# Kernel tuning notes

Hardware: AMD Instinct MI355X
Metric: run time of the kernel (lower is better)

## Reference

```python
import jax, jax.numpy as jnp
import numpy as np

N_UP, N_DOWN = 8, 8
N_ELEC = N_UP + N_DOWN
N_NUC = 4
D, K, F, H = 128, 64, 32, 45  # embedding, kernel, dist_feat, w-MLP hidden (log-spaced)
CUTOFF = 10.0
B = 2048


def _pairs(a, b):
    s, r = np.meshgrid(a, b, indexing='ij')
    return s.ravel(), r.ravel()


def _edges():
    up = np.arange(N_UP)
    dn = np.arange(N_UP, N_ELEC)
    su, ru = _pairs(up, up); m = su != ru; su, ru = su[m], ru[m]
    sd, rd = _pairs(dn, dn); m = sd != rd; sd, rd = sd[m], rd[m]
    same_s = np.concatenate([su, sd]); same_r = np.concatenate([ru, rd])
    a1s, a1r = _pairs(up, dn); a2s, a2r = _pairs(dn, up)
    anti_s = np.concatenate([a1s, a2s]); anti_r = np.concatenate([a1r, a2r])
    ne_s = np.repeat(np.arange(N_NUC), N_ELEC)
    ne_r = np.tile(np.arange(N_ELEC), N_NUC)
    return tuple(jnp.asarray(x, jnp.int32) for x in (same_s, same_r, anti_s, anti_r, ne_s, ne_r))


def setup_inputs() -> dict:
    key = jax.random.key(0)
    ks = jax.random.split(key, 10)
    rs = jax.random.normal(ks[0], (B, N_ELEC, 3)) * 2.0
    coords = jax.random.normal(ks[1], (N_NUC, 3)) * 2.0
    X_tab = jax.random.normal(ks[2], (1, D))
    Y_w = jax.random.normal(ks[3], (N_NUC, K)) / np.sqrt(N_NUC)
    wW1 = jax.random.normal(ks[4], (3, 3, F, H)) / np.sqrt(F)
    wb1 = jax.random.normal(ks[5], (3, 3, H)) * 0.1
    wW2 = jax.random.normal(ks[6], (3, 3, H, K)) / np.sqrt(H)
    h0_tab = jax.random.normal(ks[7], (2, 1, K))
    hW = jax.random.normal(ks[8], (2, 2, D, K)) / np.sqrt(D)
    gW = jax.random.normal(ks[9], (3, 3, K, D)) / np.sqrt(K)
    same_s, same_r, anti_s, anti_r, ne_s, ne_r = _edges()
    return dict(rs=rs, coords=coords, X_tab=X_tab, Y_w=Y_w, wW1=wW1, wb1=wb1,
                wW2=wW2, h0_tab=h0_tab, hW=hW, gW=gW,
                same_s=same_s, same_r=same_r, anti_s=anti_s, anti_r=anti_r,
                ne_s=ne_s, ne_r=ne_r)


def _dist_basis(d):
    # DistanceBasis with 'nocusp' envelope: env = d^2 exp(-d), gaussians at mus
    qs = jnp.linspace(0.0, 1.0, F)
    mus = CUTOFF * qs ** 2
    sigmas = (1.0 + CUTOFF * qs) / 7.0
    env = d ** 2 * jnp.exp(-d)
    return env[..., None] * jnp.exp(-((d[..., None] - mus) ** 2) / sigmas ** 2)


def reference(rs, coords, X_tab, Y_w, wW1, wb1, wW2, h0_tab, hW, gW,
              same_s, same_r, anti_s, anti_r, ne_s, ne_r):
    Bn = rs.shape[0]
    spin_idxs = jnp.zeros((N_ELEC,), jnp.int32)  # n_up == n_down -> one spin class
    # per-edge distances (layer-0 update_edges_fn featurizes them once)
    d_same = jnp.linalg.norm(rs[:, same_s] - rs[:, same_r], axis=-1)  # [B,112]
    d_anti = jnp.linalg.norm(rs[:, anti_s] - rs[:, anti_r], axis=-1)  # [B,128]
    d_ne = jnp.linalg.norm(coords[ne_s][None] - rs[:, ne_r], axis=-1)  # [B,64]
    feats = [_dist_basis(d_same), _dist_basis(d_anti), _dist_basis(d_ne)]
    senders = [same_s, anti_s, ne_s]
    receivers = [same_r, anti_r, ne_r]
    elec = X_tab[spin_idxs]  # [N_ELEC, D] electron embedding X(spin_idxs)
    nuc = Y_w                # Y(eye(n_nuc)) == Y_w, [N_NUC, K]
    for l in range(3):
        upd = 0.0
        for j in range(3):  # same, anti, ne
            # w subnet: 2-layer MLP, silu hidden with bias, bias-free linear out
            we = jax.nn.silu(feats[j] @ wW1[l, j] + wb1[l, j]) @ wW2[l, j]  # [B,E,K]
            if j < 2:
                if l == 0:
                    hx = h0_tab[j][spin_idxs][senders[j]]            # [E,K] embed
                else:
                    hx = (elec @ hW[l - 1, j])[:, senders[j]]        # [B,E,K]
                weh = we * hx
            else:
                weh = we * nuc[ne_s][None]                           # [B,E,K]
            # segment_sum scatter into receiver electrons
            z = jnp.zeros((Bn, N_ELEC, K), we.dtype).at[:, receivers[j]].add(weh)
            upd = upd + z @ gW[l, j]                                  # [B,N_ELEC,D]
        elec = elec + upd
    return elec
```

## Files before the change

kernel.cpp:

```cpp
#include <hip/hip_runtime.h>
#include <hip/hip_bf16.h>

#define NE 16
#define NN 4
#define DDIM 128
#define KD 64
#define HD 45

typedef _Float16 half8 __attribute__((ext_vector_type(8)));
typedef _Float16 half4 __attribute__((ext_vector_type(4)));
typedef float floatx4 __attribute__((ext_vector_type(4)));

#define OFF_FLAG_B 0
#define OFF_B1_B   64
#define OFF_XT_B   1792
#define OFF_H0_B   2304
#define OFF_YW_B   2560
#define OFF_W1_B   3072
#define OFF_W2_B   30720
#define OFF_GW_B   104448
#define OFF_HW_B   251904
#define OFF_IND_B  317440

__device__ __forceinline__ float ldf(const void* p, long i, int f32) {
    if (f32) return ((const float*)p)[i];
    unsigned int u = ((unsigned int)((const unsigned short*)p)[i]) << 16;
    return __uint_as_float(u);
}

__global__ void prep2_kernel(const void* w1, const void* b1, const void* w2, const void* h0,
                             const void* hW, const void* gW, const void* Yw, const void* Xt,
                             const void* rs,
                             const int* __restrict__ same_r, const int* __restrict__ anti_r,
                             const int* __restrict__ ne_r, char* wsB) {
    __shared__ int badS;
    if (threadIdx.x == 0) badS = 0;
    __syncthreads();
    {
        const unsigned short* rs16 = (const unsigned short*)rs;
        int bad = 0;
        for (int i = threadIdx.x; i < 2048; i += 256) {
            unsigned int u = ((unsigned int)rs16[i]) << 16;
            float v = __uint_as_float(u);
            if (!(fabsf(v) < 1e6f)) bad = 1;
        }
        if (bad) atomicOr(&badS, 1);
    }
    __syncthreads();
    const int f32 = badS ? 1 : 0;
    if (blockIdx.x == 0 && threadIdx.x == 0) *(int*)(wsB + OFF_FLAG_B) = f32;

    int i = blockIdx.x * 256 + threadIdx.x;
    _Float16* W1F = (_Float16*)(wsB + OFF_W1_B);
    _Float16* W2F = (_Float16*)(wsB + OFF_W2_B);
    _Float16* GWF = (_Float16*)(wsB + OFF_GW_B);
    _Float16* HWF = (_Float16*)(wsB + OFF_HW_B);
    _Float16* INDF= (_Float16*)(wsB + OFF_IND_B);
    float*    B1  = (float*)(wsB + OFF_B1_B);
    float*    XT  = (float*)(wsB + OFF_XT_B);
    _Float16* H0F = (_Float16*)(wsB + OFF_H0_B);
    _Float16* YWF = (_Float16*)(wsB + OFF_YW_B);

    if (i < 13824) {
        int lj = i / 1536, rem = i % 1536;
        int nt = rem >> 9, lane = (rem & 511) >> 3, e = rem & 7;
        int row = ((lane >> 4) << 3) + e;
        int col = (nt << 4) + (lane & 15);
        W1F[i] = (_Float16)((col < 45) ? ldf(w1, lj * 1440 + row * 45 + col, f32) : 0.f);
    }
    if (i < 36864) {
        int lj = i / 4096, rem = i & 4095;
        int nt = rem >> 10, kt = (rem >> 9) & 1, lane = (rem & 511) >> 3, e = rem & 7;
        int row = (kt << 5) + ((lane >> 4) << 3) + e;
        int col = (nt << 4) + (lane & 15);
        W2F[i] = (_Float16)((row < 45) ? ldf(w2, lj * 2880 + row * 64 + col, f32) : 0.f);
    }
    if (i < 73728) {
        int lj = i >> 13, rem = i & 8191;
        int nt = rem >> 10, kt = (rem >> 9) & 1, lane = (rem & 511) >> 3, e = rem & 7;
        int row = (kt << 5) + ((lane >> 4) << 3) + e;
        int col = (nt << 4) + (lane & 15);
        GWF[i] = (_Float16)ldf(gW, lj * 8192 + row * 128 + col, f32);
    }
    if (i < 32768) {
        int lj = i >> 13, rem = i & 8191;
        int nt = rem >> 11, kt = (rem >> 9) & 3, lane = (rem & 511) >> 3, e = rem & 7;
        int row = (kt << 5) + ((lane >> 4) << 3) + e;
        int col = (nt << 4) + (lane & 15);
        HWF[i] = (_Float16)ldf(hW, lj * 8192 + row * 64 + col, f32);
    }
    if (i < 5120) {
        int c = i >> 9, rem = i & 511;
        int ln = rem >> 3, ii = rem & 7;
        int cls = (c < 4) ? 0 : ((c < 8) ? 1 : 2);
        int lc  = c - ((cls == 0) ? 0 : ((cls == 1) ? 4 : 8));
        int qd = ln >> 4, lm = ln & 15;
        int e = lc * 32 + qd * 8 + ii;
        int cnt = (cls == 0) ? 112 : ((cls == 1) ? 128 : 64);
        int r = 255;
        if (e < cnt) r = (cls == 0) ? same_r[e] : ((cls == 1) ? anti_r[e] : ne_r[e]);
        INDF[i] = (r == lm) ? (_Float16)1.0f : (_Float16)0.0f;
    }
    if (i < 432) { int lj = i / 48, n = i % 48; B1[i] = (n < 45) ? ldf(b1, lj * 45 + n, f32) : 0.f; }
    if (i < 128) XT[i] = ldf(Xt, i, f32);
    if (i < 128) H0F[i] = (_Float16)ldf(h0, i, f32);
    if (i < 256) YWF[i] = (_Float16)ldf(Yw, i, f32);
}

__device__ __forceinline__ half8 feat_tile(
    const void* __restrict__ rs, const void* __restrict__ coords,
    int b, int lm, int f32, int tloc, int cls,
    const int* __restrict__ S, const int* __restrict__ R,
    const float* __restrict__ A0, const float* __restrict__ B0, const float* __restrict__ C0)
{
    int le = tloc * 16 + lm;
    int s = S[le], r = R[le];
    long rb = ((long)b * NE + r) * 3;
    float bx = ldf(rs, rb + 0, f32), by = ldf(rs, rb + 1, f32), bz = ldf(rs, rb + 2, f32);
    float ax, ay, az;
    if (cls < 2) {
        long sb = ((long)b * NE + s) * 3;
        ax = ldf(rs, sb + 0, f32); ay = ldf(rs, sb + 1, f32); az = ldf(rs, sb + 2, f32);
    } else {
        ax = ldf(coords, s * 3 + 0, f32); ay = ldf(coords, s * 3 + 1, f32); az = ldf(coords, s * 3 + 2, f32);
    }
    float dx = ax - bx, dy = ay - by, dz = az - bz;
    float d = sqrtf(dx * dx + dy * dy + dz * dz);
    float d2 = d * d;
    half8 a;
    #pragma unroll
    for (int ii = 0; ii < 8; ++ii) {
        float E = fmaf(A0[ii], d2, fmaf(B0[ii], d, C0[ii]));
        a[ii] = (_Float16)(d2 * __expf(E));
    }
    return a;
}

__device__ __forceinline__ void we_tile_weh(
    half8 fa, int lj, int tile,
    const char* __restrict__ wsB, _Float16* __restrict__ hid,
    const _Float16* __restrict__ hxrow,
    const unsigned char* __restrict__ sendC,
    _Float16* __restrict__ wehT,
    int lane, int qd, int lm)
{
    const half8* W1F_lj = (const half8*)(wsB + OFF_W1_B) + lj * 192;
    half8 w0 = W1F_lj[lane], w1v = W1F_lj[64 + lane], w2v = W1F_lj[128 + lane];
    const float* B1 = (const float*)(wsB + OFF_B1_B) + lj * 48;
    float bi0 = B1[lm], bi1 = B1[16 + lm], bi2 = B1[32 + lm];
    floatx4 c0 = {0.f,0.f,0.f,0.f}, c1 = c0, c2 = c0;
    c0 = __builtin_amdgcn_mfma_f32_16x16x32_f16(fa, w0,  c0, 0, 0, 0);
    c1 = __builtin_amdgcn_mfma_f32_16x16x32_f16(fa, w1v, c1, 0, 0, 0);
    c2 = __builtin_amdgcn_mfma_f32_16x16x32_f16(fa, w2v, c2, 0, 0, 0);
    #pragma unroll
    for (int rr = 0; rr < 4; ++rr) {
        int row = qd * 4 + rr;
        int x = (row & 7) << 4;
        float v0 = c0[rr] + bi0, v1 = c1[rr] + bi1, v2 = c2[rr] + bi2;
        v0 = v0 * __builtin_amdgcn_rcpf(1.f + __expf(-v0));
        v1 = v1 * __builtin_amdgcn_rcpf(1.f + __expf(-v1));
        v2 = v2 * __builtin_amdgcn_rcpf(1.f + __expf(-v2));
        char* hb = (char*)hid + row * 128;
        *(_Float16*)(hb + ((lm * 2)      ^ x)) = (_Float16)v0;
        *(_Float16*)(hb + ((32 + lm * 2) ^ x)) = (_Float16)v1;
        *(_Float16*)(hb + ((64 + lm * 2) ^ x)) = (_Float16)v2;
    }
    int xr = (lm & 7) << 4;
    half8 a0 = *(const half8*)((const char*)hid + lm * 128 + ((qd * 16)      ^ xr));
    half8 a1 = *(const half8*)((const char*)hid + lm * 128 + ((64 + qd * 16) ^ xr));

    int sv0 = sendC[tile * 16 + qd * 4 + 0];
    int sv1 = sendC[tile * 16 + qd * 4 + 1];
    int sv2 = sendC[tile * 16 + qd * 4 + 2];
    int sv3 = sendC[tile * 16 + qd * 4 + 3];

    const half8* W2F_lj = (const half8*)(wsB + OFF_W2_B) + lj * 512;
    #pragma unroll
    for (int nt = 0; nt < 4; ++nt) {
        half8 bk0 = W2F_lj[nt * 128 + lane], bk1 = W2F_lj[nt * 128 + 64 + lane];
        floatx4 acc = {0.f,0.f,0.f,0.f};
        acc = __builtin_amdgcn_mfma_f32_16x16x32_f16(a0, bk0, acc, 0, 0, 0);
        acc = __builtin_amdgcn_mfma_f32_16x16x32_f16(a1, bk1, acc, 0, 0, 0);
        const int kc = nt * 16 + lm;
        const int eb = tile * 16 + qd * 4;
        wehT[kc * 136 + eb + 0] = (_Float16)(acc[0] * (float)hxrow[sv0 * 68 + kc]);
        wehT[kc * 136 + eb + 1] = (_Float16)(acc[1] * (float)hxrow[sv1 * 68 + kc]);
        wehT[kc * 136 + eb + 2] = (_Float16)(acc[2] * (float)hxrow[sv2 * 68 + kc]);
        wehT[kc * 136 + eb + 3] = (_Float16)(acc[3] * (float)hxrow[sv3 * 68 + kc]);
    }
}

__device__ __forceinline__ void z_mfma4(
    const _Float16* __restrict__ wehT, const half8* __restrict__ INDF, int c0,
    _Float16* __restrict__ zh, int wv, int qd, int lm, int lane)
{
    const _Float16* base = wehT + (wv * 16 + lm) * 136 + qd * 8;
    floatx4 zD = {0.f,0.f,0.f,0.f};
    zD = __builtin_amdgcn_mfma_f32_16x16x32_f16(*(const half8*)(base +  0), INDF[(c0 + 0) * 64 + lane], zD, 0, 0, 0);
    zD = __builtin_amdgcn_mfma_f32_16x16x32_f16(*(const half8*)(base + 32), INDF[(c0 + 1) * 64 + lane], zD, 0, 0, 0);
    zD = __builtin_amdgcn_mfma_f32_16x16x32_f16(*(const half8*)(base + 64), INDF[(c0 + 2) * 64 + lane], zD, 0, 0, 0);
    zD = __builtin_amdgcn_mfma_f32_16x16x32_f16(*(const half8*)(base + 96), INDF[(c0 + 3) * 64 + lane], zD, 0, 0, 0);
    half4 h;
    #pragma unroll
    for (int i = 0; i < 4; ++i) h[i] = (_Float16)zD[i];
    *(half4*)(zh + lm * 72 + wv * 16 + qd * 4) = h;
}

__device__ __forceinline__ void z_mfma2(
    const _Float16* __restrict__ wehT, const half8* __restrict__ INDF, int c0,
    _Float16* __restrict__ zh, int wv, int qd, int lm, int lane)
{
    const _Float16* base = wehT + (wv * 16 + lm) * 136 + qd * 8;
    floatx4 zD = {0.f,0.f,0.f,0.f};
    zD = __builtin_amdgcn_mfma_f32_16x16x32_f16(*(const half8*)(base +  0), INDF[(c0 + 0) * 64 + lane], zD, 0, 0, 0);
    zD = __builtin_amdgcn_mfma_f32_16x16x32_f16(*(const half8*)(base + 32), INDF[(c0 + 1) * 64 + lane], zD, 0, 0, 0);
    half4 h;
    #pragma unroll
    for (int i = 0; i < 4; ++i) h[i] = (_Float16)zD[i];
    *(half4*)(zh + lm * 72 + wv * 16 + qd * 4) = h;
}

__device__ __forceinline__ void gw_accum(
    int L, int j, int wv, int lane, int qd, int lm,
    const _Float16* __restrict__ zh, const half8* __restrict__ GWF, floatx4 (&eacc)[2])
{
    half8 zf0 = *(const half8*)(zh + lm * 72 + qd * 8);
    half8 zf1 = *(const half8*)(zh + lm * 72 + 32 + qd * 8);
    const half8* G = GWF + (size_t)(L * 3 + j) * 1024;
    #pragma unroll
    for (int u = 0; u < 2; ++u) {
        int t2 = wv * 2 + u;
        eacc[u] = __builtin_amdgcn_mfma_f32_16x16x32_f16(zf0, G[t2 * 128 + lane],      eacc[u], 0, 0, 0);
        eacc[u] = __builtin_amdgcn_mfma_f32_16x16x32_f16(zf1, G[t2 * 128 + 64 + lane], eacc[u], 0, 0, 0);
    }
}

__global__ __launch_bounds__(256, 2)
void fused_kernel(const void* __restrict__ rs, const void* __restrict__ coords,
                  const int* __restrict__ same_s, const int* __restrict__ same_r,
                  const int* __restrict__ anti_s, const int* __restrict__ anti_r,
                  const int* __restrict__ ne_s,   const int* __restrict__ ne_r,
                  const char* __restrict__ wsB, void* __restrict__ out)
{
    const int b = blockIdx.x;
    const int tid = threadIdx.x;
    const int wv = tid >> 6, lane = tid & 63;
    const int qd = lane >> 4, lm = lane & 15;
    const int f32 = *(const int*)(wsB + OFF_FLAG_B);

    __shared__ __align__(16) _Float16 wehT[64 * 136];
    __shared__ __align__(16) _Float16 hidA[4][1024];
    __shared__ __align__(16) _Float16 zhS[16 * 72];
    __shared__ _Float16 hxS[2 * 1088];
    __shared__ _Float16 nucS[4 * 68];
    __shared__ __align__(16) _Float16 elecB[16 * 136];
    __shared__ unsigned char sendPad[384];

    const _Float16* H0F = (const _Float16*)(wsB + OFF_H0_B);
    const _Float16* YWF = (const _Float16*)(wsB + OFF_YW_B);
    const float*    XT  = (const float*)(wsB + OFF_XT_B);
    const half8*    GWF = (const half8*)(wsB + OFF_GW_B);
    const half8*    HWF = (const half8*)(wsB + OFF_HW_B);
    const half8*    INDF= (const half8*)(wsB + OFF_IND_B);

    for (int i = tid; i < 384; i += 256) {
        int cls = i >> 7, pos = i & 127;
        int cnt = (cls == 0) ? 112 : ((cls == 1) ? 128 : 64);
        int s = 0;
        if (pos < cnt) {
            if (cls == 0)      s = same_s[pos];
            else if (cls == 1) s = anti_s[pos];
            else               s = ne_s[pos];
        }
        sendPad[i] = (unsigned char)s;
    }
    for (int i = tid; i < 2048; i += 256)
        hxS[(i >> 10) * 1088 + ((i >> 6) & 15) * 68 + (i & 63)] = H0F[((i >> 10) << 6) + (i & 63)];
    if (tid < 256) nucS[(tid >> 6) * 68 + (tid & 63)] = YWF[tid];
    for (int i = tid; i < 4352; i += 256) ((unsigned int*)wehT)[i] = 0u;
    {
        _Float16* hid = hidA[wv];
        half8 z8 = {0,0,0,0,0,0,0,0};
        *(half8*)(hid + lane * 8) = z8;
        *(half8*)(hid + 512 + lane * 8) = z8;
    }
    __syncthreads();

    half8 fa_s0, fa_s1 = {0,0,0,0,0,0,0,0}, fa_a0, fa_a1, fa_n;
    {
        float A0[8], B0[8], C0[8];
        #pragma unroll
        for (int ii = 0; ii < 8; ++ii) {
            float qf = (float)(qd * 8 + ii) * (1.f / 31.f);
            float mu = 10.f * qf * qf;
            float u = 7.f * __builtin_amdgcn_rcpf(1.f + 10.f * qf);
            float is2 = u * u;
            A0[ii] = -is2;
            B0[ii] = 2.f * mu * is2 - 1.f;
            C0[ii] = -(mu * mu) * is2;
        }
        fa_s0 = feat_tile(rs, coords, b, lm, f32, wv,     0, same_s, same_r, A0, B0, C0);
        if (wv < 3)
        fa_s1 = feat_tile(rs, coords, b, lm, f32, wv + 4, 0, same_s, same_r, A0, B0, C0);
        fa_a0 = feat_tile(rs, coords, b, lm, f32, wv,     1, anti_s, anti_r, A0, B0, C0);
        fa_a1 = feat_tile(rs, coords, b, lm, f32, wv + 4, 1, anti_s, anti_r, A0, B0, C0);
        fa_n  = feat_tile(rs, coords, b, lm, f32, wv,     2, ne_s,   ne_r,   A0, B0, C0);
    }

    floatx4 eacc[2];
    #pragma unroll
    for (int u = 0; u < 2; ++u) {
        float xv = XT[(wv * 2 + u) * 16 + lm];
        eacc[u][0] = xv; eacc[u][1] = xv; eacc[u][2] = xv; eacc[u][3] = xv;
    }

    _Float16* hid = hidA[wv];

    for (int L = 0; L < 3; ++L) {
        const int lj0 = L * 3;
        we_tile_weh(fa_s0, lj0, wv, wsB, hid, hxS, sendPad, wehT, lane, qd, lm);
        if (wv < 3)
        we_tile_weh(fa_s1, lj0, wv + 4, wsB, hid, hxS, sendPad, wehT, lane, qd, lm);
        __syncthreads();
        z_mfma4(wehT, INDF, 0, zhS, wv, qd, lm, lane);
        __syncthreads();
        gw_accum(L, 0, wv, lane, qd, lm, zhS, GWF, eacc);
        we_tile_weh(fa_a0, lj0 + 1, wv,     wsB, hid, hxS + 1088, sendPad + 128, wehT, lane, qd, lm);
        we_tile_weh(fa_a1, lj0 + 1, wv + 4, wsB, hid, hxS + 1088, sendPad + 128, wehT, lane, qd, lm);
        __syncthreads();
        z_mfma4(wehT, INDF, 4, zhS, wv, qd, lm, lane);
        __syncthreads();
        gw_accum(L, 1, wv, lane, qd, lm, zhS, GWF, eacc);
        we_tile_weh(fa_n, lj0 + 2, wv, wsB, hid, nucS, sendPad + 256, wehT, lane, qd, lm);
        __syncthreads();
        z_mfma2(wehT, INDF, 8, zhS, wv, qd, lm, lane);
        __syncthreads();
        gw_accum(L, 2, wv, lane, qd, lm, zhS, GWF, eacc);

        if (L < 2) {
            #pragma unroll
            for (int u = 0; u < 2; ++u) {
                int t2 = wv * 2 + u;
                #pragma unroll
                for (int r = 0; r < 4; ++r)
                    elecB[(qd * 4 + r) * 136 + t2 * 16 + lm] = (_Float16)eacc[u][r];
            }
            __syncthreads();
            half8 ae[4];
            #pragma unroll
            for (int kt = 0; kt < 4; ++kt)
                ae[kt] = *(const half8*)(elecB + lm * 136 + kt * 32 + qd * 8);
            #pragma unroll
            for (int u = 0; u < 2; ++u) {
                int idx = wv * 2 + u;
                int j = idx >> 2, nt = idx & 3;
                floatx4 acc = {0.f,0.f,0.f,0.f};
                #pragma unroll
                for (int kt = 0; kt < 4; ++kt) {
                    half8 g = HWF[(size_t)(((L * 2 + j) * 4 + nt) * 4 + kt) * 64 + lane];
                    acc = __builtin_amdgcn_mfma_f32_16x16x32_f16(ae[kt], g, acc, 0, 0, 0);
                }
                #pragma unroll
                for (int r = 0; r < 4; ++r)
                    hxS[j * 1088 + (qd * 4 + r) * 68 + nt * 16 + lm] = (_Float16)acc[r];
            }
            __syncthreads();
        }
    }

    if (f32) {
        float* o = (float*)out + (size_t)b * 2048;
        #pragma unroll
        for (int u = 0; u < 2; ++u)
            #pragma unroll
            for (int r = 0; r < 4; ++r)
                o[(qd * 4 + r) * 128 + (wv * 2 + u) * 16 + lm] = eacc[u][r];
    } else {
        __hip_bfloat16* o = (__hip_bfloat16*)out + (size_t)b * 2048;
        #pragma unroll
        for (int u = 0; u < 2; ++u)
            #pragma unroll
            for (int r = 0; r < 4; ++r)
                o[(qd * 4 + r) * 128 + (wv * 2 + u) * 16 + lm] = __float2bfloat16(eacc[u][r]);
    }
}

extern "C" void kernel_launch(void* const* d_in, const int* in_sizes, int n_in,
                              void* d_out, int out_size, void* d_ws, size_t ws_size,
                              hipStream_t stream) {
    const void* rs     = d_in[0];
    const void* coords = d_in[1];
    const void* X_tab  = d_in[2];
    const void* Y_w    = d_in[3];
    const void* wW1    = d_in[4];
    const void* wb1    = d_in[5];
    const void* wW2    = d_in[6];
    const void* h0     = d_in[7];
    const void* hW     = d_in[8];
    const void* gW     = d_in[9];
    const int* same_s = (const int*)d_in[10];
    const int* same_r = (const int*)d_in[11];
    const int* anti_s = (const int*)d_in[12];
    const int* anti_r = (const int*)d_in[13];
    const int* ne_s   = (const int*)d_in[14];
    const int* ne_r   = (const int*)d_in[15];
    char* wsB = (char*)d_ws;

    const int Bn = in_sizes[0] / (NE * 3);

    prep2_kernel<<<288, 256, 0, stream>>>(wW1, wb1, wW2, h0, hW, gW, Y_w, X_tab, rs,
                                          same_r, anti_r, ne_r, wsB);
    fused_kernel<<<Bn, 256, 0, stream>>>(rs, coords, same_s, same_r, anti_s, anti_r,
                                         ne_s, ne_r, wsB, d_out);
}
```

Before: 187.0 us.

## Pack hidden and hx operands as half2, fold bias into MFMA accumulator

The MLP bias is now loaded into the MFMA accumulator as its initial value, so the separate bias add goes away. The three silu outputs per row are written to LDS as one packed 8-byte store, which needs the W2 weight rows permuted to match the new interleaved hidden layout. The hx and nucleus tables are stored as packed half2 pairs (k and k+32) with stride 33. This lets the weh product use packed fp16 multiplies and 64-bit LDS stores instead of scalar loads and 16-bit stores. It trades fp32 multiplies for fp16 precision in the we*hx product and adds bit-shuffling ALU work.

```diff
diff --git a/kernel.cpp b/kernel.cpp
--- a/kernel.cpp
+++ b/kernel.cpp
@@ -9,6 +9,8 @@
 
 typedef _Float16 half8 __attribute__((ext_vector_type(8)));
 typedef _Float16 half4 __attribute__((ext_vector_type(4)));
+typedef __fp16 half2v __attribute__((ext_vector_type(2)));
+typedef unsigned uint2v __attribute__((ext_vector_type(2)));
 typedef float floatx4 __attribute__((ext_vector_type(4)));
 
 #define OFF_FLAG_B 0
@@ -71,9 +73,10 @@
     if (i < 36864) {
         int lj = i / 4096, rem = i & 4095;
         int nt = rem >> 10, kt = (rem >> 9) & 1, lane = (rem & 511) >> 3, e = rem & 7;
-        int row = (kt << 5) + ((lane >> 4) << 3) + e;
+        int q = (kt << 5) + ((lane >> 4) << 3) + e;
+        int hsel = q & 3, hrow = hsel * 16 + (q >> 2);
         int col = (nt << 4) + (lane & 15);
-        W2F[i] = (_Float16)((row < 45) ? ldf(w2, lj * 2880 + row * 64 + col, f32) : 0.f);
+        W2F[i] = (_Float16)((hsel < 3 && hrow < 45) ? ldf(w2, lj * 2880 + hrow * 64 + col, f32) : 0.f);
     }
     if (i < 73728) {
         int lj = i >> 13, rem = i & 8191;
@@ -139,7 +142,7 @@
 __device__ __forceinline__ void we_tile_weh(
     half8 fa, int lj, int tile,
     const char* __restrict__ wsB, _Float16* __restrict__ hid,
-    const _Float16* __restrict__ hxrow,
+    const unsigned* __restrict__ hxP,
     const unsigned char* __restrict__ sendC,
     _Float16* __restrict__ wehT,
     int lane, int qd, int lm)
@@ -148,45 +151,69 @@
     half8 w0 = W1F_lj[lane], w1v = W1F_lj[64 + lane], w2v = W1F_lj[128 + lane];
     const float* B1 = (const float*)(wsB + OFF_B1_B) + lj * 48;
     float bi0 = B1[lm], bi1 = B1[16 + lm], bi2 = B1[32 + lm];
-    floatx4 c0 = {0.f,0.f,0.f,0.f}, c1 = c0, c2 = c0;
+    floatx4 c0 = {bi0, bi0, bi0, bi0};
+    floatx4 c1 = {bi1, bi1, bi1, bi1};
+    floatx4 c2 = {bi2, bi2, bi2, bi2};
     c0 = __builtin_amdgcn_mfma_f32_16x16x32_f16(fa, w0,  c0, 0, 0, 0);
     c1 = __builtin_amdgcn_mfma_f32_16x16x32_f16(fa, w1v, c1, 0, 0, 0);
     c2 = __builtin_amdgcn_mfma_f32_16x16x32_f16(fa, w2v, c2, 0, 0, 0);
     #pragma unroll
     for (int rr = 0; rr < 4; ++rr) {
         int row = qd * 4 + rr;
-        int x = (row & 7) << 4;
-        float v0 = c0[rr] + bi0, v1 = c1[rr] + bi1, v2 = c2[rr] + bi2;
+        float v0 = c0[rr], v1 = c1[rr], v2 = c2[rr];
         v0 = v0 * __builtin_amdgcn_rcpf(1.f + __expf(-v0));
         v1 = v1 * __builtin_amdgcn_rcpf(1.f + __expf(-v1));
         v2 = v2 * __builtin_amdgcn_rcpf(1.f + __expf(-v2));
-        char* hb = (char*)hid + row * 128;
-        *(_Float16*)(hb + ((lm * 2)      ^ x)) = (_Float16)v0;
-        *(_Float16*)(hb + ((32 + lm * 2) ^ x)) = (_Float16)v1;
-        *(_Float16*)(hb + ((64 + lm * 2) ^ x)) = (_Float16)v2;
+        half2v plo = __builtin_amdgcn_cvt_pkrtz(v0, v1);
+        half2v phi = __builtin_amdgcn_cvt_pkrtz(v2, 0.f);
+        uint2v pk;
+        pk[0] = __builtin_bit_cast(unsigned, plo);
+        pk[1] = __builtin_bit_cast(unsigned, phi);
+        *(uint2v*)((char*)hid + row * 128 + ((lm * 8) ^ ((row & 7) << 4))) = pk;
     }
     int xr = (lm & 7) << 4;
     half8 a0 = *(const half8*)((const char*)hid + lm * 128 + ((qd * 16)      ^ xr));
     half8 a1 = *(const half8*)((const char*)hid + lm * 128 + ((64 + qd * 16) ^ xr));
 
-    int sv0 = sendC[tile * 16 + qd * 4 + 0];
-    int sv1 = sendC[tile * 16 + qd * 4 + 1];
-    int sv2 = sendC[tile * 16 + qd * 4 + 2];
-    int sv3 = sendC[tile * 16 + qd * 4 + 3];
+    unsigned svw = *(const unsigned*)(sendC + tile * 16 + qd * 4);
+    int sv0 = svw & 255, sv1 = (svw >> 8) & 255, sv2 = (svw >> 16) & 255, sv3 = svw >> 24;
 
     const half8* W2F_lj = (const half8*)(wsB + OFF_W2_B) + lj * 512;
-    #pragma unroll
-    for (int nt = 0; nt < 4; ++nt) {
-        half8 bk0 = W2F_lj[nt * 128 + lane], bk1 = W2F_lj[nt * 128 + 64 + lane];
-        floatx4 acc = {0.f,0.f,0.f,0.f};
-        acc = __builtin_amdgcn_mfma_f32_16x16x32_f16(a0, bk0, acc, 0, 0, 0);
-        acc = __builtin_amdgcn_mfma_f32_16x16x32_f16(a1, bk1, acc, 0, 0, 0);
-        const int kc = nt * 16 + lm;
-        const int eb = tile * 16 + qd * 4;
-        wehT[kc * 136 + eb + 0] = (_Float16)(acc[0] * (float)hxrow[sv0 * 68 + kc]);
-        wehT[kc * 136 + eb + 1] = (_Float16)(acc[1] * (float)hxrow[sv1 * 68 + kc]);
-        wehT[kc * 136 + eb + 2] = (_Float16)(acc[2] * (float)hxrow[sv2 * 68 + kc]);
-        wehT[kc * 136 + eb + 3] = (_Float16)(acc[3] * (float)hxrow[sv3 * 68 + kc]);
+    floatx4 acc0 = {0.f,0.f,0.f,0.f}, acc1 = acc0, acc2 = acc0, acc3 = acc0;
+    acc0 = __builtin_amdgcn_mfma_f32_16x16x32_f16(a0, W2F_lj[      lane], acc0, 0, 0, 0);
+    acc0 = __builtin_amdgcn_mfma_f32_16x16x32_f16(a1, W2F_lj[ 64 + lane], acc0, 0, 0, 0);
+    acc1 = __builtin_amdgcn_mfma_f32_16x16x32_f16(a0, W2F_lj[128 + lane], acc1, 0, 0, 0);
+    acc1 = __builtin_amdgcn_mfma_f32_16x16x32_f16(a1, W2F_lj[192 + lane], acc1, 0, 0, 0);
+    acc2 = __builtin_amdgcn_mfma_f32_16x16x32_f16(a0, W2F_lj[256 + lane], acc2, 0, 0, 0);
+    acc2 = __builtin_amdgcn_mfma_f32_16x16x32_f16(a1, W2F_lj[320 + lane], acc2, 0, 0, 0);
+    acc3 = __builtin_amdgcn_mfma_f32_16x16x32_f16(a0, W2F_lj[384 + lane], acc3, 0, 0, 0);
+    acc3 = __builtin_amdgcn_mfma_f32_16x16x32_f16(a1, W2F_lj[448 + lane], acc3, 0, 0, 0);
+
+    const int eb = tile * 16 + qd * 4;
+    #pragma unroll
+    for (int p = 0; p < 2; ++p) {
+        unsigned ha = hxP[sv0 * 33 + p * 16 + lm];
+        unsigned hb = hxP[sv1 * 33 + p * 16 + lm];
+        unsigned hc = hxP[sv2 * 33 + p * 16 + lm];
+        unsigned hd = hxP[sv3 * 33 + p * 16 + lm];
+        floatx4 aL = p ? acc1 : acc0;
+        floatx4 aH = p ? acc3 : acc2;
+        half2v m0h = __builtin_amdgcn_cvt_pkrtz(aL[0], aH[0]) * __builtin_bit_cast(half2v, ha);
+        half2v m1h = __builtin_amdgcn_cvt_pkrtz(aL[1], aH[1]) * __builtin_bit_cast(half2v, hb);
+        half2v m2h = __builtin_amdgcn_cvt_pkrtz(aL[2], aH[2]) * __builtin_bit_cast(half2v, hc);
+        half2v m3h = __builtin_amdgcn_cvt_pkrtz(aL[3], aH[3]) * __builtin_bit_cast(half2v, hd);
+        unsigned m0 = __builtin_bit_cast(unsigned, m0h);
+        unsigned m1 = __builtin_bit_cast(unsigned, m1h);
+        unsigned m2 = __builtin_bit_cast(unsigned, m2h);
+        unsigned m3 = __builtin_bit_cast(unsigned, m3h);
+        uint2v lo, hi;
+        lo[0] = (m0 & 0xFFFFu) | (m1 << 16);
+        lo[1] = (m2 & 0xFFFFu) | (m3 << 16);
+        hi[0] = (m0 >> 16) | (m1 & 0xFFFF0000u);
+        hi[1] = (m2 >> 16) | (m3 & 0xFFFF0000u);
+        const int klo = p * 16 + lm;
+        *(uint2v*)(wehT + klo * 136 + eb) = lo;
+        *(uint2v*)(wehT + (klo + 32) * 136 + eb) = hi;
     }
 }
 
@@ -251,8 +278,8 @@
     __shared__ __align__(16) _Float16 wehT[64 * 136];
     __shared__ __align__(16) _Float16 hidA[4][1024];
     __shared__ __align__(16) _Float16 zhS[16 * 72];
-    __shared__ _Float16 hxS[2 * 1088];
-    __shared__ _Float16 nucS[4 * 68];
+    __shared__ unsigned hxPall[2 * 528];
+    __shared__ unsigned nucP[4 * 33];
     __shared__ __align__(16) _Float16 elecB[16 * 136];
     __shared__ unsigned char sendPad[384];
 
@@ -274,16 +301,19 @@
         }
         sendPad[i] = (unsigned char)s;
     }
-    for (int i = tid; i < 2048; i += 256)
-        hxS[(i >> 10) * 1088 + ((i >> 6) & 15) * 68 + (i & 63)] = H0F[((i >> 10) << 6) + (i & 63)];
-    if (tid < 256) nucS[(tid >> 6) * 68 + (tid & 63)] = YWF[tid];
+    for (int t = tid; t < 1024; t += 256) {
+        int j = t >> 9, rem = t & 511, s = rem >> 5, i = rem & 31;
+        unsigned lo = ((const unsigned short*)H0F)[j * 64 + i];
+        unsigned hi = ((const unsigned short*)H0F)[j * 64 + 32 + i];
+        hxPall[j * 528 + s * 33 + i] = lo | (hi << 16);
+    }
+    if (tid < 128) {
+        int s = tid >> 5, i = tid & 31;
+        unsigned lo = ((const unsigned short*)YWF)[s * 64 + i];
+        unsigned hi = ((const unsigned short*)YWF)[s * 64 + 32 + i];
+        nucP[s * 33 + i] = lo | (hi << 16);
+    }
     for (int i = tid; i < 4352; i += 256) ((unsigned int*)wehT)[i] = 0u;
-    {
-        _Float16* hid = hidA[wv];
-        half8 z8 = {0,0,0,0,0,0,0,0};
-        *(half8*)(hid + lane * 8) = z8;
-        *(half8*)(hid + 512 + lane * 8) = z8;
-    }
     __syncthreads();
 
     half8 fa_s0, fa_s1 = {0,0,0,0,0,0,0,0}, fa_a0, fa_a1, fa_n;
@@ -318,20 +348,20 @@
 
     for (int L = 0; L < 3; ++L) {
         const int lj0 = L * 3;
-        we_tile_weh(fa_s0, lj0, wv, wsB, hid, hxS, sendPad, wehT, lane, qd, lm);
+        we_tile_weh(fa_s0, lj0, wv, wsB, hid, hxPall, sendPad, wehT, lane, qd, lm);
         if (wv < 3)
-        we_tile_weh(fa_s1, lj0, wv + 4, wsB, hid, hxS, sendPad, wehT, lane, qd, lm);
+        we_tile_weh(fa_s1, lj0, wv + 4, wsB, hid, hxPall, sendPad, wehT, lane, qd, lm);
         __syncthreads();
         z_mfma4(wehT, INDF, 0, zhS, wv, qd, lm, lane);
         __syncthreads();
         gw_accum(L, 0, wv, lane, qd, lm, zhS, GWF, eacc);
-        we_tile_weh(fa_a0, lj0 + 1, wv,     wsB, hid, hxS + 1088, sendPad + 128, wehT, lane, qd, lm);
-        we_tile_weh(fa_a1, lj0 + 1, wv + 4, wsB, hid, hxS + 1088, sendPad + 128, wehT, lane, qd, lm);
+        we_tile_weh(fa_a0, lj0 + 1, wv,     wsB, hid, hxPall + 528, sendPad + 128, wehT, lane, qd, lm);
+        we_tile_weh(fa_a1, lj0 + 1, wv + 4, wsB, hid, hxPall + 528, sendPad + 128, wehT, lane, qd, lm);
         __syncthreads();
         z_mfma4(wehT, INDF, 4, zhS, wv, qd, lm, lane);
         __syncthreads();
         gw_accum(L, 1, wv, lane, qd, lm, zhS, GWF, eacc);
-        we_tile_weh(fa_n, lj0 + 2, wv, wsB, hid, nucS, sendPad + 256, wehT, lane, qd, lm);
+        we_tile_weh(fa_n, lj0 + 2, wv, wsB, hid, nucP, sendPad + 256, wehT, lane, qd, lm);
         __syncthreads();
         z_mfma2(wehT, INDF, 8, zhS, wv, qd, lm, lane);
         __syncthreads();
@@ -346,23 +376,29 @@
                     elecB[(qd * 4 + r) * 136 + t2 * 16 + lm] = (_Float16)eacc[u][r];
             }
             __syncthreads();
-            half8 ae[4];
-            #pragma unroll
-            for (int kt = 0; kt < 4; ++kt)
-                ae[kt] = *(const half8*)(elecB + lm * 136 + kt * 32 + qd * 8);
-            #pragma unroll
-            for (int u = 0; u < 2; ++u) {
-                int idx = wv * 2 + u;
-                int j = idx >> 2, nt = idx & 3;
-                floatx4 acc = {0.f,0.f,0.f,0.f};
+            {
+                half8 ae0 = *(const half8*)(elecB + lm * 136 +  0 + qd * 8);
+                half8 ae1 = *(const half8*)(elecB + lm * 136 + 32 + qd * 8);
+                half8 ae2 = *(const half8*)(elecB + lm * 136 + 64 + qd * 8);
+                half8 ae3 = *(const half8*)(elecB + lm * 136 + 96 + qd * 8);
+                _Float16* hp = (_Float16*)hxPall;
                 #pragma unroll
-                for (int kt = 0; kt < 4; ++kt) {
-                    half8 g = HWF[(size_t)(((L * 2 + j) * 4 + nt) * 4 + kt) * 64 + lane];
-                    acc = __builtin_amdgcn_mfma_f32_16x16x32_f16(ae[kt], g, acc, 0, 0, 0);
+                for (int u = 0; u < 2; ++u) {
+                    int idx = wv * 2 + u;
+                    int j = idx >> 2, nt = idx & 3;
+                    const half8* Bb = HWF + (size_t)(((L * 2 + j) * 4 + nt) * 4) * 64;
+                    floatx4 acc = {0.f,0.f,0.f,0.f};
+                    acc = __builtin_amdgcn_mfma_f32_16x16x32_f16(ae0, Bb[  0 + lane], acc, 0, 0, 0);
+                    acc = __builtin_amdgcn_mfma_f32_16x16x32_f16(ae1, Bb[ 64 + lane], acc, 0, 0, 0);
+                    acc = __builtin_amdgcn_mfma_f32_16x16x32_f16(ae2, Bb[128 + lane], acc, 0, 0, 0);
+                    acc = __builtin_amdgcn_mfma_f32_16x16x32_f16(ae3, Bb[192 + lane], acc, 0, 0, 0);
+                    const int k = nt * 16 + lm;
+                    #pragma unroll
+                    for (int r = 0; r < 4; ++r) {
+                        int s = qd * 4 + r;
+                        hp[(j * 528 + s * 33 + (k & 31)) * 2 + (k >> 5)] = (_Float16)acc[r];
+                    }
                 }
-                #pragma unroll
-                for (int r = 0; r < 4; ++r)
-                    hxS[j * 1088 + (qd * 4 + r) * 68 + nt * 16 + lm] = (_Float16)acc[r];
             }
             __syncthreads();
         }
```

Result: no change. 184.1 us, median of 2 (-1.6%).
